# Optimization experiments

Hardware: AMD Instinct MI355X
Metric: run time of the kernel (lower is better)

The kernel has to match this reference:

```python
import jax, jax.numpy as jnp
import numpy as np

N_NODES = 20000
N_EDGES = 200000
D_MODEL = 128
N_HEADS = 8
N_LAYERS = 2  # num_gnn - 1 concat layers


def setup_inputs() -> dict:
    key = jax.random.key(0)
    ks = jax.random.split(key, 12)
    s = 0.05  # keep activations well-scaled across residual layers
    hd = D_MODEL // N_HEADS  # 16
    return {
        "x": jax.random.normal(ks[0], (N_NODES, D_MODEL), jnp.float32),
        "src": jax.random.randint(ks[1], (N_EDGES,), 0, N_NODES),
        "dst": jax.random.randint(ks[2], (N_EDGES,), 0, N_NODES),
        "Ws": jax.random.normal(ks[3], (N_LAYERS, D_MODEL, D_MODEL), jnp.float32) * s,
        "als": jax.random.normal(ks[4], (N_LAYERS, N_HEADS, hd), jnp.float32) * s,
        "ars": jax.random.normal(ks[5], (N_LAYERS, N_HEADS, hd), jnp.float32) * s,
        "bs": jax.random.normal(ks[6], (N_LAYERS, D_MODEL), jnp.float32) * s,
        "W_last": jax.random.normal(ks[7], (D_MODEL, N_HEADS * D_MODEL), jnp.float32) * s,
        "al_last": jax.random.normal(ks[8], (N_HEADS, D_MODEL), jnp.float32) * s,
        "ar_last": jax.random.normal(ks[9], (N_HEADS, D_MODEL), jnp.float32) * s,
        "b_last": jax.random.normal(ks[10], (N_HEADS * D_MODEL,), jnp.float32) * s,
    }


def gat_conv(h, src, dst, W, al, ar, b, num_nodes):
    """DGL GATConv (eval mode, dropout off): returns (N, H, D) head outputs."""
    H, D = al.shape
    feat = (h @ W).reshape(num_nodes, H, D)          # (N,H,D)
    el = jnp.sum(feat * al[None], axis=-1)           # (N,H) attn on src side
    er = jnp.sum(feat * ar[None], axis=-1)           # (N,H) attn on dst side
    e = jax.nn.leaky_relu(el[src] + er[dst], 0.2)    # (E,H)
    # edge softmax over incoming edges of each dst node, per head
    m = jax.ops.segment_max(e, dst, num_segments=num_nodes)  # (N,H)
    p = jnp.exp(e - m[dst])                          # (E,H)
    z = jax.ops.segment_sum(p, dst, num_segments=num_nodes)  # (N,H)
    a = p / z[dst]                                   # (E,H)
    msg = feat[src] * a[..., None]                   # (E,H,D) weighted messages
    rst = jax.ops.segment_sum(msg, dst, num_segments=num_nodes)  # (N,H,D)
    return rst + b.reshape(1, H, D)


def reference(x, src, dst, Ws, als, ars, bs, W_last, al_last, ar_last, b_last):
    N = x.shape[0]
    h = x
    for i in range(N_LAYERS):
        temp = gat_conv(h, src, dst, Ws[i], als[i], ars[i], bs[i], N)  # (N,H,hd)
        h = h + jax.nn.elu(temp.reshape(N, -1))       # concat heads, ELU, residual
    temp = gat_conv(h, src, dst, W_last, al_last, ar_last, b_last, N)  # (N,H,D)
    h = h + jnp.mean(temp, axis=1)                    # mean over heads, residual
    return h
```

## Files before the change

kernel.cpp:

```cpp
#include <hip/hip_runtime.h>
#include <math.h>

#define N_NODES 20000
#define N_EDGES 200000
#define DM 128
#define NH 8

typedef __attribute__((ext_vector_type(8))) short bf16x8;
typedef __attribute__((ext_vector_type(4))) float f32x4;

__device__ __forceinline__ unsigned short f2b(float f) {
  unsigned int u = __float_as_uint(f);
  unsigned int r = (u + 0x7FFFu + ((u >> 16) & 1u)) >> 16;
  return (unsigned short)r;
}
__device__ __forceinline__ float b2f(unsigned short s) {
  return __uint_as_float(((unsigned int)s) << 16);
}

__global__ __launch_bounds__(256) void degzero(int* __restrict__ deg) {
  int i = blockIdx.x * 256 + threadIdx.x;
  if (i < N_NODES) deg[i] = 0;
}

__global__ __launch_bounds__(256) void prep_all(
    const float* __restrict__ x, float* __restrict__ h, unsigned short* __restrict__ hb,
    const int* __restrict__ dstE, int* __restrict__ deg, int* __restrict__ rank,
    const float* __restrict__ Ws, unsigned short* __restrict__ wsz,
    const float* __restrict__ W_last, unsigned short* __restrict__ wpsz,
    const float* __restrict__ al_last, const float* __restrict__ ar_last,
    const float* __restrict__ b_last, unsigned short* __restrict__ wlrsz,
    float* __restrict__ mb) {
  int i = blockIdx.x * 256 + threadIdx.x;
  if (i < (N_NODES * DM) / 4) {
    float4 v = ((const float4*)x)[i];
    ((float4*)h)[i] = v;
    ((ushort4*)hb)[i] = make_ushort4(f2b(v.x), f2b(v.y), f2b(v.z), f2b(v.w));
  }
  if (i < N_EDGES) rank[i] = atomicAdd(&deg[dstE[i]], 1);
  if (i < 2 * 16384) {
    int layer = i >> 14;
    int r = i & 16383;
    int j = r & 7, l = (r >> 3) & 63, f = (r >> 9) & 7, ks = r >> 12;
    int k = ks * 32 + ((l >> 4) << 3) + j;
    int n = f * 16 + (l & 15);
    wsz[i] = f2b(Ws[(size_t)layer * 16384 + k * 128 + n]);
  }
  if (i < 131072) {
    int j = i & 7, l = (i >> 3) & 63, f = (i >> 9) & 7, ks = i >> 12;
    int k = ks * 32 + ((l >> 4) << 3) + j;
    int n = f * 16 + (l & 15);
    int h_ = k >> 7, ko = k & 127;
    wpsz[i] = f2b(W_last[(size_t)ko * 1024 + h_ * 128 + n] * 0.125f);
  }
  if (i < 2048) {
    int j = i & 7, l = (i >> 3) & 63, ks = i >> 9;
    int k = ks * 32 + ((l >> 4) << 3) + j;
    int n = l & 15;
    int hh = n & 7;
    const float* av = (n < 8) ? (al_last + hh * 128) : (ar_last + hh * 128);
    float s = 0.f;
    for (int d = 0; d < 128; ++d) s += W_last[(size_t)k * 1024 + hh * 128 + d] * av[d];
    wlrsz[i] = f2b(s);
  }
  if (i < 128) {
    float s = 0.f;
#pragma unroll
    for (int hh = 0; hh < 8; ++hh) s += b_last[hh * 128 + i];
    mb[i] = s * 0.125f;
  }
}

__global__ void scan_deg(const int* __restrict__ deg, int* __restrict__ off,
                         int* __restrict__ perm) {
  __shared__ int part[1024];
  __shared__ int bbase[64];
  __shared__ int bcur[64];
  const int tid = threadIdx.x;
  const int CHUNK = (N_NODES + 1023) / 1024;
  int base = tid * CHUNK;
  int s = 0;
  for (int i = 0; i < CHUNK; ++i) {
    int idx = base + i;
    if (idx < N_NODES) s += deg[idx];
  }
  part[tid] = s;
  __syncthreads();
  for (int ofs = 1; ofs < 1024; ofs <<= 1) {
    int v = (tid >= ofs) ? part[tid - ofs] : 0;
    __syncthreads();
    part[tid] += v;
    __syncthreads();
  }
  int run = (tid > 0) ? part[tid - 1] : 0;
  for (int i = 0; i < CHUNK; ++i) {
    int idx = base + i;
    if (idx < N_NODES) {
      off[idx] = run;
      run += deg[idx];
    }
  }
  if (tid == 0) off[N_NODES] = part[1023];

  if (tid < 64) bcur[tid] = 0;
  __syncthreads();
  for (int i = 0; i < CHUNK; ++i) {
    int idx = base + i;
    if (idx < N_NODES) atomicAdd(&bcur[min(deg[idx], 63)], 1);
  }
  __syncthreads();
  if (tid == 0) {
    int r2 = 0;
    for (int b = 0; b < 64; ++b) {
      int c = bcur[b];
      bbase[b] = r2;
      r2 += c;
    }
  }
  __syncthreads();
  if (tid < 64) bcur[tid] = 0;
  __syncthreads();
  for (int i = 0; i < CHUNK; ++i) {
    int idx = base + i;
    if (idx < N_NODES) {
      int d = min(deg[idx], 63);
      int p = atomicAdd(&bcur[d], 1);
      perm[bbase[d] + p] = idx;
    }
  }
}

template <int K>
__device__ __forceinline__ void dev_gemm(int tile, const unsigned short* __restrict__ A,
                                         const unsigned short* __restrict__ Bsz,
                                         unsigned short* __restrict__ Cb,
                                         const float* __restrict__ al,
                                         const float* __restrict__ ar,
                                         float* __restrict__ elr, int lane, int wid) {
  const int wrow = wid & 1, wc = wid >> 1;
  const int r0 = tile * 32;
  const int arow = r0 + wrow * 16 + (lane & 15);
  const int kg = lane >> 4;

  f32x4 acc[4];
#pragma unroll
  for (int fi = 0; fi < 4; ++fi) acc[fi] = {0.f, 0.f, 0.f, 0.f};

  const bf16x8* Ap = (const bf16x8*)(A + (size_t)arow * K + kg * 8);
#pragma unroll 4
  for (int ks = 0; ks < K / 32; ++ks) {
    bf16x8 a = Ap[ks * 4];
#pragma unroll
    for (int fi = 0; fi < 4; ++fi) {
      int f = wc * 4 + fi;
      bf16x8 b = *(const bf16x8*)(Bsz + (((size_t)(ks * 8 + f) * 64 + lane) << 3));
      acc[fi] = __builtin_amdgcn_mfma_f32_16x16x32_bf16(a, b, acc[fi], 0, 0, 0);
    }
  }

  const int rbase = r0 + wrow * 16 + (lane >> 4) * 4;
#pragma unroll
  for (int fi = 0; fi < 4; ++fi) {
    int col = wc * 64 + fi * 16 + (lane & 15);
#pragma unroll
    for (int r = 0; r < 4; ++r) {
      Cb[(size_t)(rbase + r) * DM + col] = f2b(acc[fi][r]);
    }
  }

#pragma unroll
  for (int fi = 0; fi < 4; ++fi) {
    int hh = wc * 4 + fi;
    float alv = al[hh * 16 + (lane & 15)];
    float arv = ar[hh * 16 + (lane & 15)];
#pragma unroll
    for (int r = 0; r < 4; ++r) {
      float pl = acc[fi][r] * alv;
      float pr = acc[fi][r] * arv;
#pragma unroll
      for (int msk = 1; msk < 16; msk <<= 1) {
        pl += __shfl_xor(pl, msk, 64);
        pr += __shfl_xor(pr, msk, 64);
      }
      if ((lane & 15) == 0) {
        int row = rbase + r;
        elr[row * 16 + hh] = pl;
        elr[row * 16 + 8 + hh] = pr;
      }
    }
  }
}

__global__ __launch_bounds__(256) void gemm0_scatter(
    const unsigned short* __restrict__ A, const unsigned short* __restrict__ Bsz,
    unsigned short* __restrict__ Cb, const float* __restrict__ al,
    const float* __restrict__ ar, float* __restrict__ elr, const int* __restrict__ srcE,
    const int* __restrict__ dstE, const int* __restrict__ rank,
    const int* __restrict__ off, int* __restrict__ csr_src) {
  const int bid = blockIdx.x;
  if (bid < N_NODES / 32) {
    dev_gemm<DM>(bid, A, Bsz, Cb, al, ar, elr, threadIdx.x & 63, threadIdx.x >> 6);
  } else {
    int e = (bid - N_NODES / 32) * 256 + threadIdx.x;
    if (e < N_EDGES) {
      csr_src[off[dstE[e]] + rank[e]] = srcE[e];
    }
  }
}

template <int MODE>
__global__ __launch_bounds__(256) void fused_small(
    const int* __restrict__ perm, const int* __restrict__ off,
    const int* __restrict__ csr_src, const unsigned short* __restrict__ feat,
    const float* __restrict__ elr, const float* __restrict__ bias, float* __restrict__ h,
    unsigned short* __restrict__ hb, const unsigned short* __restrict__ wsz1,
    const float* __restrict__ al1, const float* __restrict__ ar1,
    unsigned short* __restrict__ feat_out, float* __restrict__ elr_out,
    const unsigned short* __restrict__ wlrsz, float* __restrict__ elr2_out) {
  __shared__ float a_lds[4][64];
  __shared__ int s_lds[4][8];
  __shared__ float zi_lds[4][8];
  __shared__ __align__(16) unsigned short nh_lds[4][128];
  __shared__ int pnode[4];
  const int wid = threadIdx.x >> 6;
  const int t = perm[blockIdx.x * 4 + wid];
  const int lane = threadIdx.x & 63;
  const int e_loc = lane >> 3, hh = lane & 7;
  const int hg = lane >> 3;
  const int beg = off[t], end = off[t + 1];
  const float ert = elr[t * 16 + 8 + hh];
  if (lane == 0) pnode[wid] = t;

  int e = beg + e_loc;
  bool val = e < end;
  int s = val ? csr_src[e] : 0;
  float xl = val ? elr[s * 16 + hh] : 0.f;

  float z = 0.f, acc0 = 0.f, acc1 = 0.f;
  for (int base = beg; base < end; base += 8) {
    float ex = 0.f;
    if (val) {
      float xv = xl + ert;
      xv = xv > 0.f ? xv : 0.2f * xv;
      ex = __expf(xv);
    }
    a_lds[wid][lane] = ex;
    if (hh == 0) s_lds[wid][e_loc] = s;
    __builtin_amdgcn_wave_barrier();
    asm volatile("s_waitcnt lgkmcnt(0)" ::: "memory");
    z += ex;
    int en = base + 8 + e_loc;
    bool valn = en < end;
    int sn = valn ? csr_src[en] : 0;
    float xln = valn ? elr[sn * 16 + hh] : 0.f;
    int n = min(8, end - base);
    if (n == 8) {
#pragma unroll
      for (int e2 = 0; e2 < 8; ++e2) {
        int s2 = s_lds[wid][e2];
        float a = a_lds[wid][e2 * 8 + hg];
        unsigned int hv = *(const unsigned int*)&feat[(size_t)s2 * 128 + 2 * lane];
        acc0 += a * b2f((unsigned short)(hv & 0xffffu));
        acc1 += a * b2f((unsigned short)(hv >> 16));
      }
    } else {
      for (int e2 = 0; e2 < n; ++e2) {
        int s2 = s_lds[wid][e2];
        float a = a_lds[wid][e2 * 8 + hg];
        unsigned int hv = *(const unsigned int*)&feat[(size_t)s2 * 128 + 2 * lane];
        acc0 += a * b2f((unsigned short)(hv & 0xffffu));
        acc1 += a * b2f((unsigned short)(hv >> 16));
      }
    }
    __builtin_amdgcn_wave_barrier();
    s = sn;
    xl = xln;
    val = valn;
  }
  z += __shfl_xor(z, 8, 64);
  z += __shfl_xor(z, 16, 64);
  z += __shfl_xor(z, 32, 64);
  if (e_loc == 0) zi_lds[wid][hh] = (z > 0.f) ? 1.f / z : 0.f;
  __builtin_amdgcn_wave_barrier();
  asm volatile("s_waitcnt lgkmcnt(0)" ::: "memory");
  float zi = zi_lds[wid][hg];

  float2 bv = *(const float2*)&bias[2 * lane];
  float v0 = acc0 * zi + bv.x;
  float v1 = acc1 * zi + bv.y;
  v0 = v0 > 0.f ? v0 : expm1f(v0);
  v1 = v1 > 0.f ? v1 : expm1f(v1);
  size_t idx = (size_t)t * 128 + 2 * lane;
  float2 hv = *(const float2*)&h[idx];
  float nh0 = hv.x + v0;
  float nh1 = hv.y + v1;
  *(float2*)&h[idx] = make_float2(nh0, nh1);
  unsigned short b0 = f2b(nh0), b1 = f2b(nh1);
  *(ushort2*)&hb[idx] = make_ushort2(b0, b1);
  *(ushort2*)&nh_lds[wid][2 * lane] = make_ushort2(b0, b1);

  if (MODE == 1) {
    __builtin_amdgcn_wave_barrier();
    asm volatile("s_waitcnt lgkmcnt(0)" ::: "memory");
    const int kg = lane >> 4;
    f32x4 acc = {0.f, 0.f, 0.f, 0.f};
#pragma unroll
    for (int ks = 0; ks < 4; ++ks) {
      bf16x8 a = *(const bf16x8*)&nh_lds[wid][ks * 32 + kg * 8];
      bf16x8 b = *(const bf16x8*)(wlrsz + (((size_t)ks * 64 + lane) << 3));
      acc = __builtin_amdgcn_mfma_f32_16x16x32_bf16(a, b, acc, 0, 0, 0);
    }
    if (lane < 16) elr2_out[t * 16 + lane] = acc[0];
  }

  if (MODE == 0) {
    __syncthreads();
    const int r16 = lane & 15;
    const int kg = lane >> 4;
    f32x4 acc2[2];
    acc2[0] = {0.f, 0.f, 0.f, 0.f};
    acc2[1] = {0.f, 0.f, 0.f, 0.f};
#pragma unroll
    for (int ks = 0; ks < 4; ++ks) {
      bf16x8 a = {0, 0, 0, 0, 0, 0, 0, 0};
      if (r16 < 4) a = *(const bf16x8*)&nh_lds[r16][ks * 32 + kg * 8];
#pragma unroll
      for (int fi = 0; fi < 2; ++fi) {
        int f = wid * 2 + fi;
        bf16x8 b = *(const bf16x8*)(wsz1 + (((size_t)(ks * 8 + f) * 64 + lane) << 3));
        acc2[fi] = __builtin_amdgcn_mfma_f32_16x16x32_bf16(a, b, acc2[fi], 0, 0, 0);
      }
    }
    const int rowl = (lane >> 4) * 4;
#pragma unroll
    for (int fi = 0; fi < 2; ++fi) {
      int f = wid * 2 + fi;
      int col = f * 16 + r16;
      float alv = al1[col];
      float arv = ar1[col];
#pragma unroll
      for (int r = 0; r < 4; ++r) {
        float v = acc2[fi][r];
        if (rowl == 0) feat_out[(size_t)pnode[r] * 128 + col] = f2b(v);
        float pl = v * alv;
        float pr = v * arv;
#pragma unroll
        for (int msk = 1; msk < 16; msk <<= 1) {
          pl += __shfl_xor(pl, msk, 64);
          pr += __shfl_xor(pr, msk, 64);
        }
        if (r16 == 0 && rowl == 0) {
          int pn = pnode[r];
          elr_out[pn * 16 + f] = pl;
          elr_out[pn * 16 + 8 + f] = pr;
        }
      }
    }
  }
}

#define GT_STRIDE 1032
__global__ __launch_bounds__(1024) void agg_gemm16(
    const int* __restrict__ perm, const int* __restrict__ off,
    const int* __restrict__ csr_src, const unsigned short* __restrict__ hb,
    const float* __restrict__ elr, const unsigned short* __restrict__ wpsz,
    const float* __restrict__ hres, const float* __restrict__ mb,
    float* __restrict__ out) {
  __shared__ __align__(16) unsigned short gt[16][GT_STRIDE];
  __shared__ float red[8][64][4];
  __shared__ float a_lds[16][64];
  __shared__ int s_lds[16][8];
  __shared__ float zi_lds[16][8];
  __shared__ int pnode[16];
  const int wid = threadIdx.x >> 6;
  const int lane = threadIdx.x & 63;
  const int t0 = blockIdx.x * 16;
  const int t = perm[t0 + wid];
  const int e_loc = lane >> 3, hh = lane & 7;
  if (lane == 0) pnode[wid] = t;

  {
    const int beg = off[t], end = off[t + 1];
    const float ert = elr[t * 16 + 8 + hh];
    int e = beg + e_loc;
    bool val = e < end;
    int s = val ? csr_src[e] : 0;
    float xl = val ? elr[s * 16 + hh] : 0.f;

    float z = 0.f;
    float accA[8], accB[8];
#pragma unroll
    for (int k = 0; k < 8; ++k) accA[k] = accB[k] = 0.f;

    for (int base = beg; base < end; base += 8) {
      float ex = 0.f;
      if (val) {
        float xv = xl + ert;
        xv = xv > 0.f ? xv : 0.2f * xv;
        ex = __expf(xv);
      }
      a_lds[wid][lane] = ex;
      if (hh == 0) s_lds[wid][e_loc] = s;
      __builtin_amdgcn_wave_barrier();
      asm volatile("s_waitcnt lgkmcnt(0)" ::: "memory");
      z += ex;
      int en = base + 8 + e_loc;
      bool valn = en < end;
      int sn = valn ? csr_src[en] : 0;
      float xln = valn ? elr[sn * 16 + hh] : 0.f;
      int n = min(8, end - base);
      if (n == 8) {
#pragma unroll
        for (int e2 = 0; e2 < 8; ++e2) {
          int s2 = s_lds[wid][e2];
          float4 pa = *(const float4*)&a_lds[wid][e2 * 8];
          float4 pb = *(const float4*)&a_lds[wid][e2 * 8 + 4];
          unsigned int hv = *(const unsigned int*)&hb[(size_t)s2 * 128 + 2 * lane];
          float h0 = b2f((unsigned short)(hv & 0xffffu));
          float h1 = b2f((unsigned short)(hv >> 16));
          accA[0] += pa.x * h0; accB[0] += pa.x * h1;
          accA[1] += pa.y * h0; accB[1] += pa.y * h1;
          accA[2] += pa.z * h0; accB[2] += pa.z * h1;
          accA[3] += pa.w * h0; accB[3] += pa.w * h1;
          accA[4] += pb.x * h0; accB[4] += pb.x * h1;
          accA[5] += pb.y * h0; accB[5] += pb.y * h1;
          accA[6] += pb.z * h0; accB[6] += pb.z * h1;
          accA[7] += pb.w * h0; accB[7] += pb.w * h1;
        }
      } else {
        for (int e2 = 0; e2 < n; ++e2) {
          int s2 = s_lds[wid][e2];
          float4 pa = *(const float4*)&a_lds[wid][e2 * 8];
          float4 pb = *(const float4*)&a_lds[wid][e2 * 8 + 4];
          unsigned int hv = *(const unsigned int*)&hb[(size_t)s2 * 128 + 2 * lane];
          float h0 = b2f((unsigned short)(hv & 0xffffu));
          float h1 = b2f((unsigned short)(hv >> 16));
          accA[0] += pa.x * h0; accB[0] += pa.x * h1;
          accA[1] += pa.y * h0; accB[1] += pa.y * h1;
          accA[2] += pa.z * h0; accB[2] += pa.z * h1;
          accA[3] += pa.w * h0; accB[3] += pa.w * h1;
          accA[4] += pb.x * h0; accB[4] += pb.x * h1;
          accA[5] += pb.y * h0; accB[5] += pb.y * h1;
          accA[6] += pb.z * h0; accB[6] += pb.z * h1;
          accA[7] += pb.w * h0; accB[7] += pb.w * h1;
        }
      }
      __builtin_amdgcn_wave_barrier();
      s = sn;
      xl = xln;
      val = valn;
    }
    z += __shfl_xor(z, 8, 64);
    z += __shfl_xor(z, 16, 64);
    z += __shfl_xor(z, 32, 64);
    if (e_loc == 0) zi_lds[wid][hh] = (z > 0.f) ? 1.f / z : 0.f;
    __builtin_amdgcn_wave_barrier();
    asm volatile("s_waitcnt lgkmcnt(0)" ::: "memory");
    float4 zia = *(const float4*)&zi_lds[wid][0];
    float4 zib = *(const float4*)&zi_lds[wid][4];
    float ziv[8] = {zia.x, zia.y, zia.z, zia.w, zib.x, zib.y, zib.z, zib.w};
#pragma unroll
    for (int h2 = 0; h2 < 8; ++h2) {
      *(ushort2*)&gt[wid][h2 * 128 + 2 * lane] =
          make_ushort2(f2b(accA[h2] * ziv[h2]), f2b(accB[h2] * ziv[h2]));
    }
  }
  __syncthreads();

  const int f = wid & 7;
  const int kh = wid >> 3;
  const int ar16 = lane & 15;
  const int kg = lane >> 4;
  f32x4 acc = {0.f, 0.f, 0.f, 0.f};
#pragma unroll 4
  for (int ksl = 0; ksl < 16; ++ksl) {
    int ks = kh * 16 + ksl;
    bf16x8 a = *(const bf16x8*)&gt[ar16][ks * 32 + kg * 8];
    bf16x8 b = *(const bf16x8*)(wpsz + (((size_t)(ks * 8 + f) * 64 + lane) << 3));
    acc = __builtin_amdgcn_mfma_f32_16x16x32_bf16(a, b, acc, 0, 0, 0);
  }
  if (kh == 1) {
    *(float4*)&red[f][lane][0] = make_float4(acc[0], acc[1], acc[2], acc[3]);
  }
  __syncthreads();
  if (kh == 0) {
    float4 p = *(const float4*)&red[f][lane][0];
    const int col = f * 16 + (lane & 15);
    const int rb = (lane >> 4) * 4;
    float r4[4] = {p.x, p.y, p.z, p.w};
#pragma unroll
    for (int r = 0; r < 4; ++r) {
      int row = pnode[rb + r];
      out[(size_t)row * 128 + col] =
          acc[r] + r4[r] + hres[(size_t)row * 128 + col] + mb[col];
    }
  }
}

extern "C" void kernel_launch(void* const* d_in, const int* in_sizes, int n_in,
                              void* d_out, int out_size, void* d_ws, size_t ws_size,
                              hipStream_t stream) {
  const float* x = (const float*)d_in[0];
  const int* src = (const int*)d_in[1];
  const int* dst = (const int*)d_in[2];
  const float* Ws = (const float*)d_in[3];
  const float* als = (const float*)d_in[4];
  const float* ars = (const float*)d_in[5];
  const float* bs = (const float*)d_in[6];
  const float* W_last = (const float*)d_in[7];
  const float* al_last = (const float*)d_in[8];
  const float* ar_last = (const float*)d_in[9];
  const float* b_last = (const float*)d_in[10];
  float* out = (float*)d_out;

  float* h = (float*)d_ws;
  float* elr0 = h + 2560000;
  float* elrB = elr0 + 320000;
  float* elr2 = elrB + 320000;
  float* mb = elr2 + 320000;
  unsigned short* hb = (unsigned short*)(mb + 128);
  unsigned short* featA = hb + 2560000;
  unsigned short* featB = featA + 2560000;
  unsigned short* wsz = featB + 2560000;
  unsigned short* wpsz = wsz + 32768;
  unsigned short* wlrsz = wpsz + 131072;
  int* deg = (int*)(wlrsz + 2048);
  int* off = deg + N_NODES;
  int* rank = off + N_NODES + 1;
  int* csr_src = rank + N_EDGES;
  int* perm = csr_src + N_EDGES;

  const int GB = N_NODES / 32;
  const int FB = N_NODES / 4;
  const int EB = (N_EDGES + 255) / 256;

  degzero<<<(N_NODES + 255) / 256, 256, 0, stream>>>(deg);
  prep_all<<<(N_NODES * DM / 4 + 255) / 256, 256, 0, stream>>>(
      x, h, hb, dst, deg, rank, Ws, wsz, W_last, wpsz, al_last, ar_last, b_last, wlrsz, mb);
  scan_deg<<<1, 1024, 0, stream>>>(deg, off, perm);
  gemm0_scatter<<<GB + EB, 256, 0, stream>>>(hb, wsz, featA, als, ars, elr0, src, dst,
                                             rank, off, csr_src);
  fused_small<0><<<FB, 256, 0, stream>>>(perm, off, csr_src, featA, elr0, bs, h, hb,
                                         wsz + 16384, als + 128, ars + 128, featB, elrB,
                                         nullptr, nullptr);
  fused_small<1><<<FB, 256, 0, stream>>>(perm, off, csr_src, featB, elrB, bs + 128, h, hb,
                                         nullptr, nullptr, nullptr, nullptr, nullptr,
                                         wlrsz, elr2);
  agg_gemm16<<<N_NODES / 16, 1024, 0, stream>>>(perm, off, csr_src, hb, elr2, wpsz, h, mb,
                                                out);
}
```

Baseline: 188.1 us.

## Move degree-bucket permutation out of single-block scan into parallel gemm0 blocks

```diff
diff --git a/kernel.cpp b/kernel.cpp
--- a/kernel.cpp
+++ b/kernel.cpp
@@ -72,17 +72,25 @@
 }
 
 __global__ void scan_deg(const int* __restrict__ deg, int* __restrict__ off,
-                         int* __restrict__ perm) {
+                         int* __restrict__ bbase_g, int* __restrict__ bcur_g) {
   __shared__ int part[1024];
-  __shared__ int bbase[64];
-  __shared__ int bcur[64];
+  __shared__ int hist[16][64];
   const int tid = threadIdx.x;
+  const int wv = tid >> 6, lane = tid & 63;
   const int CHUNK = (N_NODES + 1023) / 1024;
   int base = tid * CHUNK;
+
+  for (int i = tid; i < 16 * 64; i += 1024) ((int*)hist)[i] = 0;
+  __syncthreads();
+
   int s = 0;
   for (int i = 0; i < CHUNK; ++i) {
     int idx = base + i;
-    if (idx < N_NODES) s += deg[idx];
+    if (idx < N_NODES) {
+      int d = deg[idx];
+      s += d;
+      atomicAdd(&hist[wv][min(d, 63)], 1);
+    }
   }
   part[tid] = s;
   __syncthreads();
@@ -102,31 +110,18 @@
   }
   if (tid == 0) off[N_NODES] = part[1023];
 
-  if (tid < 64) bcur[tid] = 0;
-  __syncthreads();
-  for (int i = 0; i < CHUNK; ++i) {
-    int idx = base + i;
-    if (idx < N_NODES) atomicAdd(&bcur[min(deg[idx], 63)], 1);
-  }
-  __syncthreads();
-  if (tid == 0) {
-    int r2 = 0;
-    for (int b = 0; b < 64; ++b) {
-      int c = bcur[b];
-      bbase[b] = r2;
-      r2 += c;
-    }
-  }
-  __syncthreads();
-  if (tid < 64) bcur[tid] = 0;
-  __syncthreads();
-  for (int i = 0; i < CHUNK; ++i) {
-    int idx = base + i;
-    if (idx < N_NODES) {
-      int d = min(deg[idx], 63);
-      int p = atomicAdd(&bcur[d], 1);
-      perm[bbase[d] + p] = idx;
-    }
+  if (wv == 0) {
+    int c = 0;
+#pragma unroll
+    for (int w = 0; w < 16; ++w) c += hist[w][lane];
+    int inc = c;
+#pragma unroll
+    for (int ofs = 1; ofs < 64; ofs <<= 1) {
+      int v = __shfl_up(inc, ofs, 64);
+      if (lane >= ofs) inc += v;
+    }
+    bbase_g[lane] = inc - c;
+    bcur_g[lane] = 0;
   }
 }
 
@@ -196,14 +191,24 @@
     unsigned short* __restrict__ Cb, const float* __restrict__ al,
     const float* __restrict__ ar, float* __restrict__ elr, const int* __restrict__ srcE,
     const int* __restrict__ dstE, const int* __restrict__ rank,
-    const int* __restrict__ off, int* __restrict__ csr_src) {
+    const int* __restrict__ off, int* __restrict__ csr_src, const int* __restrict__ deg,
+    const int* __restrict__ bbase_g, int* __restrict__ bcur_g, int* __restrict__ perm) {
   const int bid = blockIdx.x;
-  if (bid < N_NODES / 32) {
+  const int GB = N_NODES / 32;
+  const int EB = (N_EDGES + 255) / 256;
+  if (bid < GB) {
     dev_gemm<DM>(bid, A, Bsz, Cb, al, ar, elr, threadIdx.x & 63, threadIdx.x >> 6);
-  } else {
-    int e = (bid - N_NODES / 32) * 256 + threadIdx.x;
+  } else if (bid < GB + EB) {
+    int e = (bid - GB) * 256 + threadIdx.x;
     if (e < N_EDGES) {
       csr_src[off[dstE[e]] + rank[e]] = srcE[e];
+    }
+  } else {
+    int idx = (bid - GB - EB) * 256 + threadIdx.x;
+    if (idx < N_NODES) {
+      int d = min(deg[idx], 63);
+      int p = atomicAdd(&bcur_g[d], 1);
+      perm[bbase_g[d] + p] = idx;
     }
   }
 }
@@ -529,17 +534,21 @@
   int* rank = off + N_NODES + 1;
   int* csr_src = rank + N_EDGES;
   int* perm = csr_src + N_EDGES;
+  int* bbase_g = perm + N_NODES;
+  int* bcur_g = bbase_g + 64;
 
   const int GB = N_NODES / 32;
   const int FB = N_NODES / 4;
   const int EB = (N_EDGES + 255) / 256;
+  const int PB = (N_NODES + 255) / 256;
 
   degzero<<<(N_NODES + 255) / 256, 256, 0, stream>>>(deg);
   prep_all<<<(N_NODES * DM / 4 + 255) / 256, 256, 0, stream>>>(
       x, h, hb, dst, deg, rank, Ws, wsz, W_last, wpsz, al_last, ar_last, b_last, wlrsz, mb);
-  scan_deg<<<1, 1024, 0, stream>>>(deg, off, perm);
-  gemm0_scatter<<<GB + EB, 256, 0, stream>>>(hb, wsz, featA, als, ars, elr0, src, dst,
-                                             rank, off, csr_src);
+  scan_deg<<<1, 1024, 0, stream>>>(deg, off, bbase_g, bcur_g);
+  gemm0_scatter<<<GB + EB + PB, 256, 0, stream>>>(hb, wsz, featA, als, ars, elr0, src,
+                                                  dst, rank, off, csr_src, deg, bbase_g,
+                                                  bcur_g, perm);
   fused_small<0><<<FB, 256, 0, stream>>>(perm, off, csr_src, featA, elr0, bs, h, hb,
                                          wsz + 16384, als + 128, ars + 128, featB, elrB,
                                          nullptr, nullptr);
```

Result: slower. 230.0 us (+22.2%).
